# Optimization experiments

Measured on AMD Instinct MI355X. Metric: run time of the kernel, lower is better.

Reference implementation:

```python
import jax, jax.numpy as jnp
import numpy as np

B, C, H, I = 32, 8, 512, 512


def act(x):
    # CustomActivation == hardtanh: (|x+1| - |x-1|) / 2
    return (jnp.abs(x + 1.0) - jnp.abs(x - 1.0)) * 0.5


def setup_inputs() -> dict:
    key = jax.random.key(0)
    ks = jax.random.split(key, 12)
    inp = jax.random.normal(ks[0], (B, C, H, I), dtype=jnp.float32)
    p_mask = jax.random.normal(ks[1], (H, I), dtype=jnp.float32)
    # Wp: tril(randn) with diagonal filled to 1 (matches __init__ + the no_grad
    # tril/clamp projection in forward, which is a no-op right after init).
    Wp = jnp.tril(jax.random.normal(ks[2], (H, H), dtype=jnp.float32))
    Wp = Wp - jnp.diag(jnp.diag(Wp)) + jnp.eye(H, dtype=jnp.float32)
    Wp_diag = jnp.ones((H,), dtype=jnp.float32)
    Wzp = jax.random.normal(ks[3], (H, H), dtype=jnp.float32)
    s = 1.0 / np.sqrt(I)
    def lin(k):
        kw, kb = jax.random.split(k)
        W = jax.random.uniform(kw, (I, I), jnp.float32, -s, s)
        b = jax.random.uniform(kb, (I,), jnp.float32, -s, s)
        return W, b
    p_lin_w, p_lin_b = lin(ks[4])
    z_lin_w, z_lin_b = lin(ks[5])
    fc1_w, fc1_b = lin(ks[6])
    fc2_w, fc2_b = lin(ks[7])
    return {
        'input': inp, 'p_mask': p_mask, 'Wp': Wp, 'Wp_diag': Wp_diag, 'Wzp': Wzp,
        'p_lin_w': p_lin_w, 'p_lin_b': p_lin_b,
        'z_lin_w': z_lin_w, 'z_lin_b': z_lin_b,
        'fc1_w': fc1_w, 'fc1_b': fc1_b, 'fc2_w': fc2_w, 'fc2_b': fc2_b,
    }


def reference(input, p_mask, Wp, Wp_diag, Wzp,
              p_lin_w, p_lin_b, z_lin_w, z_lin_b,
              fc1_w, fc1_b, fc2_w, fc2_b):
    x = input * (1.0 / 5000.0)                      # [B,C,H,I]
    p_set = x * act(p_mask)                         # split_input, broadcast over B,C
    Wp_eff = Wp + jnp.diag(Wp_diag)                 # [H,H]
    # per-channel Wp @ p_set[c], batched over B and C in one GEMM
    tp = jnp.einsum('hk,bcki->bchi', Wp_eff, p_set)
    tp = act(act(tp) @ p_lin_w.T + p_lin_b)         # p_output_layer
    tz = jnp.einsum('hk,bchi->bchi', Wzp, tp)       # wait-free channel-batched GEMM
    tz = act(act(tz) @ z_lin_w.T + z_lin_b)         # z_output_layer
    # sum over in_channel (out_channel==1 so broadcast-accumulate == sum)
    combined = tp.sum(axis=1) + tz.sum(axis=1) + x[:, 0]  # [B,H,I]
    out = jax.nn.relu(combined @ fc1_w.T + fc1_b)
    out = out @ fc2_w.T + fc2_b
    return out
```

## Files before the change

### kernel.cpp

```cpp
#include <hip/hip_runtime.h>

namespace {

constexpr int Bn = 32, Cn = 8, Hn = 512, In = 512;
constexpr size_t HI = (size_t)Hn * In;
constexpr float SC = 1.0f / 5000.0f;

using s16x8 = __attribute__((ext_vector_type(8))) short;
using f32x4 = __attribute__((ext_vector_type(4))) float;

__device__ __forceinline__ float actf(float x) {
    return fminf(1.0f, fmaxf(-1.0f, x));
}

__device__ __forceinline__ unsigned short f2bf(float f) {
    unsigned u = __builtin_bit_cast(unsigned, f);
    u += 0x7FFFu + ((u >> 16) & 1u);
    return (unsigned short)(u >> 16);
}
__device__ __forceinline__ float bf2f(unsigned short h) {
    return __builtin_bit_cast(float, (unsigned)h << 16);
}

__device__ __forceinline__ void async16(const void* g, void* l) {
    __builtin_amdgcn_global_load_lds(
        (const __attribute__((address_space(1))) unsigned*)g,
        (__attribute__((address_space(3))) unsigned*)l, 16, 0, 0);
}

template<int EPI, bool PCOL, bool TRI>
__global__ __launch_bounds__(256, 3) void mfma_gemm(
    const unsigned short* __restrict__ A,
    const unsigned short* __restrict__ Bt,
    const float* __restrict__ bias,
    const float* __restrict__ zrow,
    unsigned short* __restrict__ out0,
    unsigned short* __restrict__ out1,
    float* __restrict__ outf,
    size_t sB, size_t sC)
{
    __shared__ __align__(16) unsigned short As[128 * 32];
    __shared__ __align__(16) unsigned short Bs[128 * 32];

    const int tid  = threadIdx.x;
    const int wid  = tid >> 6, lane = tid & 63;
    const int wr   = wid >> 1, wc = wid & 1;

    const int bid = blockIdx.x;
    const int p = ((bid >> 5) << 3) | (bid & 7);
    const int q = (bid >> 3) & 3;
    const int rt = PCOL ? q : p;
    const int ct = PCOL ? (p & 3) : q;
    const size_t zb = PCOL ? (size_t)(p >> 2) : 0;

    const char* Ab = (const char*)A + (size_t)rt * 131072;
    const char* Bb = (const char*)(Bt + zb * sB) + (size_t)ct * 131072;

    f32x4 acc[4][4] = {};

    const int o0  = tid * 16;
    const int r0s = o0 >> 6;
    const int c0s = o0 & 63;

    const int kSteps = TRI ? (rt + 1) * 4 : 16;

    for (int ks = 0; ks < kSteps; ++ks) {
        const int k0b = ks * 64;
        async16(Ab + (size_t)r0s * 1024 + k0b + c0s,        (char*)As + wid * 1024);
        async16(Ab + (size_t)(64 + r0s) * 1024 + k0b + c0s, (char*)As + 4096 + wid * 1024);
        async16(Bb + (size_t)r0s * 1024 + k0b + c0s,        (char*)Bs + wid * 1024);
        async16(Bb + (size_t)(64 + r0s) * 1024 + k0b + c0s, (char*)Bs + 4096 + wid * 1024);
        __syncthreads();

        s16x8 a[4], b[4];
        const int kc = (lane >> 4) * 16;
        const int ar = wr * 64 + (lane & 15);
        const int br = wc * 64 + (lane & 15);
        #pragma unroll
        for (int m = 0; m < 4; ++m)
            a[m] = *(const s16x8*)((const char*)As + (size_t)(ar + m * 16) * 64 + kc);
        #pragma unroll
        for (int n = 0; n < 4; ++n)
            b[n] = *(const s16x8*)((const char*)Bs + (size_t)(br + n * 16) * 64 + kc);
        #pragma unroll
        for (int m = 0; m < 4; ++m)
            #pragma unroll
            for (int n = 0; n < 4; ++n)
                acc[m][n] = __builtin_amdgcn_mfma_f32_16x16x32_bf16(a[m], b[n], acc[m][n], 0, 0, 0);
        __syncthreads();
    }

    const int cb = ct * 128 + wc * 64 + (lane & 15);
    const int rb = rt * 128 + wr * 64 + ((lane >> 4) << 2);
    #pragma unroll
    for (int m = 0; m < 4; ++m) {
        #pragma unroll
        for (int n = 0; n < 4; ++n) {
            const int c = cb + n * 16;
            #pragma unroll
            for (int j = 0; j < 4; ++j) {
                const int r = rb + m * 16 + j;
                float v = acc[m][n][j];
                const size_t idx = zb * sC + (size_t)r * 512 + c;
                if (EPI == 0) {
                    out0[idx] = f2bf(actf(v));
                } else if (EPI == 1) {
                    float tp = actf(v + bias[c]);
                    out0[idx] = f2bf(tp);
                    out1[idx] = f2bf(actf(zrow[r & 511] * tp));
                } else if (EPI == 2) {
                    out0[idx] = f2bf(actf(v + bias[c]));
                } else if (EPI == 3) {
                    out0[idx] = f2bf(fmaxf(v + bias[c], 0.0f));
                } else {
                    outf[idx] = v + bias[c];
                }
            }
        }
    }
}

__global__ __launch_bounds__(256) void reduce_both(
    const unsigned short* __restrict__ tp,
    const unsigned short* __restrict__ tz,
    const float* __restrict__ x0,
    unsigned short* __restrict__ comb)
{
    size_t idx = (size_t)blockIdx.x * 256 + threadIdx.x;
    size_t b = idx >> 16;
    size_t p = (idx & 65535) * 4;
    float4 xv = *(const float4*)&x0[(b * Cn) * HI + p];
    float s0 = xv.x * SC, s1 = xv.y * SC, s2 = xv.z * SC, s3 = xv.w * SC;
    #pragma unroll
    for (int c = 0; c < Cn; ++c) {
        size_t q = (b * Cn + c) * HI + p;
        ushort4 a = *(const ushort4*)&tp[q];
        ushort4 d = *(const ushort4*)&tz[q];
        s0 += bf2f(a.x) + bf2f(d.x);
        s1 += bf2f(a.y) + bf2f(d.y);
        s2 += bf2f(a.z) + bf2f(d.z);
        s3 += bf2f(a.w) + bf2f(d.w);
    }
    ushort4 o;
    o.x = f2bf(s0); o.y = f2bf(s1); o.z = f2bf(s2); o.w = f2bf(s3);
    *(ushort4*)&comb[b * HI + p] = o;
}

__global__ __launch_bounds__(256) void transpose_mask(
    const float* __restrict__ x, const float* __restrict__ mask,
    unsigned short* __restrict__ xst)
{
    __shared__ float t[64][65];
    const int bc = blockIdx.z;
    const int i0 = blockIdx.x * 64, k0 = blockIdx.y * 64;
    const int r4 = threadIdx.x >> 6, cc = threadIdx.x & 63;
    const float* xp = x + (size_t)bc * HI;
    #pragma unroll
    for (int it = 0; it < 16; ++it) {
        int kl = it * 4 + r4;
        size_t g = (size_t)(k0 + kl) * In + i0 + cc;
        t[kl][cc] = xp[g] * (actf(mask[g]) * SC);
    }
    __syncthreads();
    unsigned short* op = xst + (size_t)bc * HI;
    #pragma unroll
    for (int it = 0; it < 16; ++it) {
        int il = it * 4 + r4;
        op[(size_t)(i0 + il) * Hn + k0 + cc] = f2bf(t[cc][il]);
    }
}

__global__ __launch_bounds__(256) void prep_wpe_bf(
    const float* __restrict__ Wp, const float* __restrict__ Wpd,
    unsigned short* __restrict__ o)
{
    int idx = blockIdx.x * 256 + threadIdx.x;
    int i = idx >> 9, j = idx & 511;
    o[idx] = f2bf(Wp[idx] + (i == j ? Wpd[i] : 0.0f));
}

__global__ __launch_bounds__(256) void conv_bf(
    const float* __restrict__ s, unsigned short* __restrict__ o)
{
    int idx = blockIdx.x * 256 + threadIdx.x;
    o[idx] = f2bf(s[idx]);
}

__global__ __launch_bounds__(64) void rowsum(
    const float* __restrict__ W, float* __restrict__ zr)
{
    int h = blockIdx.x, l = threadIdx.x;
    float s = 0.0f;
    for (int k = l; k < Hn; k += 64) s += W[h * Hn + k];
    #pragma unroll
    for (int off = 32; off; off >>= 1) s += __shfl_down(s, off, 64);
    if (!l) zr[h] = s;
}

}

extern "C" void kernel_launch(void* const* d_in, const int* in_sizes, int n_in,
                              void* d_out, int out_size, void* d_ws, size_t ws_size,
                              hipStream_t stream)
{
    const float* input  = (const float*)d_in[0];
    const float* p_mask = (const float*)d_in[1];
    const float* Wp     = (const float*)d_in[2];
    const float* Wpd    = (const float*)d_in[3];
    const float* Wzp    = (const float*)d_in[4];
    const float* plw    = (const float*)d_in[5];
    const float* plb    = (const float*)d_in[6];
    const float* zlw    = (const float*)d_in[7];
    const float* zlb    = (const float*)d_in[8];
    const float* f1w    = (const float*)d_in[9];
    const float* f1b    = (const float*)d_in[10];
    const float* f2w    = (const float*)d_in[11];
    const float* f2b    = (const float*)d_in[12];

    constexpr size_t WB = 512 * 512 * 2;
    char* w = (char*)d_ws;
    auto alloc = [&](size_t bytes) { char* p = w; w += (bytes + 255) & ~255ull; return p; };

    unsigned short* Wpeb  = (unsigned short*)alloc(WB);
    unsigned short* plwb  = (unsigned short*)alloc(WB);
    unsigned short* zlwb  = (unsigned short*)alloc(WB);
    unsigned short* f1wb  = (unsigned short*)alloc(WB);
    unsigned short* f2wb  = (unsigned short*)alloc(WB);
    float*          zrw   = (float*)alloc(512 * 4);
    unsigned short* combb = (unsigned short*)alloc((size_t)Bn * HI * 2);
    unsigned short* out1  = (unsigned short*)alloc((size_t)Bn * HI * 2);

    size_t fixedB = (size_t)(w - (char*)d_ws);
    int chunk = 32;
    while (chunk > 1 &&
           fixedB + 4ull * (size_t)chunk * Cn * HI * 2 + 4096 > ws_size)
        chunk >>= 1;
    const size_t CB = (size_t)chunk * Cn * HI * 2;
    unsigned short* xst   = (unsigned short*)alloc(CB);
    unsigned short* tpact = (unsigned short*)alloc(CB);
    unsigned short* tpb   = (unsigned short*)alloc(CB);
    unsigned short* tzin  = (unsigned short*)alloc(CB);
    unsigned short* tzb   = xst;

    prep_wpe_bf<<<512 * 512 / 256, 256, 0, stream>>>(Wp, Wpd, Wpeb);
    conv_bf<<<1024, 256, 0, stream>>>(plw, plwb);
    conv_bf<<<1024, 256, 0, stream>>>(zlw, zlwb);
    conv_bf<<<1024, 256, 0, stream>>>(f1w, f1wb);
    conv_bf<<<1024, 256, 0, stream>>>(f2w, f2wb);
    rowsum<<<512, 64, 0, stream>>>(Wzp, zrw);

    for (int b0 = 0; b0 < Bn; b0 += chunk) {
        const int nc = chunk * Cn;
        const float* inp_c = input + (size_t)b0 * Cn * HI;

        transpose_mask<<<dim3(8, 8, nc), 256, 0, stream>>>(inp_c, p_mask, xst);
        mfma_gemm<0, true, true><<<nc * 16, 256, 0, stream>>>(
            Wpeb, xst, nullptr, nullptr, tpact, nullptr, nullptr, HI, HI);
        mfma_gemm<1, false, false><<<nc * 16, 256, 0, stream>>>(
            tpact, plwb, plb, zrw, tpb, tzin, nullptr, 0, 0);
        mfma_gemm<2, false, false><<<nc * 16, 256, 0, stream>>>(
            tzin, zlwb, zlb, nullptr, tzb, nullptr, nullptr, 0, 0);
        reduce_both<<<chunk * 256, 256, 0, stream>>>(
            tpb, tzb, inp_c, combb + (size_t)b0 * HI);
    }

    mfma_gemm<3, false, false><<<512, 256, 0, stream>>>(
        combb, f1wb, f1b, nullptr, out1, nullptr, nullptr, 0, 0);
    mfma_gemm<4, false, false><<<512, 256, 0, stream>>>(
        out1, f2wb, f2b, nullptr, nullptr, nullptr, (float*)d_out, 0, 0);
}
```

Measured before the change: 564.3 us.

## Double-buffer LDS tiles in MFMA GEMM and relayout for conflict-free reads

Replaces the single-buffered load/sync/compute loop with two LDS buffers. The next K-step's async global-to-LDS loads are issued before the current step's MFMAs, and the kernel waits with an explicit vmcnt(0) plus a barrier. The LDS layout changes to K-chunk-major 16-byte rows, so each fragment read is contiguous per lane quarter, which should reduce bank conflicts. LDS use doubles to 32KB per block, which may limit occupancy under launch_bounds(256,3). The loop steps two K-steps at a time, so it relies on kSteps being even.

Measured after the change: 728.3 us. 29.1% more time.

```diff
diff --git a/kernel.cpp b/kernel.cpp
--- a/kernel.cpp
+++ b/kernel.cpp
@@ -27,6 +27,8 @@
         (const __attribute__((address_space(1))) unsigned*)g,
         (__attribute__((address_space(3))) unsigned*)l, 16, 0, 0);
 }
+
+#define VMCNT0 asm volatile("s_waitcnt vmcnt(0)" ::: "memory")
 
 template<int EPI, bool PCOL, bool TRI>
 __global__ __launch_bounds__(256, 3) void mfma_gemm(
@@ -39,12 +41,13 @@
     float* __restrict__ outf,
     size_t sB, size_t sC)
 {
-    __shared__ __align__(16) unsigned short As[128 * 32];
-    __shared__ __align__(16) unsigned short Bs[128 * 32];
+    __shared__ __align__(16) char lds0[16384];
+    __shared__ __align__(16) char lds1[16384];
 
     const int tid  = threadIdx.x;
     const int wid  = tid >> 6, lane = tid & 63;
     const int wr   = wid >> 1, wc = wid & 1;
+    const int l15  = lane & 15, kq = lane >> 4;
 
     const int bid = blockIdx.x;
     const int p = ((bid >> 5) << 3) | (bid & 7);
@@ -58,40 +61,52 @@
 
     f32x4 acc[4][4] = {};
 
-    const int o0  = tid * 16;
-    const int r0s = o0 >> 6;
-    const int c0s = o0 & 63;
-
-    const int kSteps = TRI ? (rt + 1) * 4 : 16;
-
-    for (int ks = 0; ks < kSteps; ++ks) {
-        const int k0b = ks * 64;
-        async16(Ab + (size_t)r0s * 1024 + k0b + c0s,        (char*)As + wid * 1024);
-        async16(Ab + (size_t)(64 + r0s) * 1024 + k0b + c0s, (char*)As + 4096 + wid * 1024);
-        async16(Bb + (size_t)r0s * 1024 + k0b + c0s,        (char*)Bs + wid * 1024);
-        async16(Bb + (size_t)(64 + r0s) * 1024 + k0b + c0s, (char*)Bs + 4096 + wid * 1024);
-        __syncthreads();
-
+    const size_t ro = (size_t)(tid & 127) * 1024;
+    const int    hi16 = (tid >> 7) * 16;
+    auto stage_ab = [&](char* buf, int k0b) {
+        const int kb = k0b + hi16;
+        async16(Ab + ro + kb,      buf + tid * 16);
+        async16(Ab + ro + kb + 32, buf + 4096 + tid * 16);
+        async16(Bb + ro + kb,      buf + 8192 + tid * 16);
+        async16(Bb + ro + kb + 32, buf + 12288 + tid * 16);
+    };
+
+    auto compute = [&](const char* buf) {
         s16x8 a[4], b[4];
-        const int kc = (lane >> 4) * 16;
-        const int ar = wr * 64 + (lane & 15);
-        const int br = wc * 64 + (lane & 15);
+        const int ko = kq * 2048;
         #pragma unroll
         for (int m = 0; m < 4; ++m)
-            a[m] = *(const s16x8*)((const char*)As + (size_t)(ar + m * 16) * 64 + kc);
+            a[m] = *(const s16x8*)(buf + ko + (wr * 64 + m * 16 + l15) * 16);
         #pragma unroll
         for (int n = 0; n < 4; ++n)
-            b[n] = *(const s16x8*)((const char*)Bs + (size_t)(br + n * 16) * 64 + kc);
+            b[n] = *(const s16x8*)(buf + 8192 + ko + (wc * 64 + n * 16 + l15) * 16);
         #pragma unroll
         for (int m = 0; m < 4; ++m)
             #pragma unroll
             for (int n = 0; n < 4; ++n)
                 acc[m][n] = __builtin_amdgcn_mfma_f32_16x16x32_bf16(a[m], b[n], acc[m][n], 0, 0, 0);
-        __syncthreads();
-    }
-
-    const int cb = ct * 128 + wc * 64 + (lane & 15);
-    const int rb = rt * 128 + wr * 64 + ((lane >> 4) << 2);
+    };
+
+    const int kSteps = TRI ? (rt + 1) * 4 : 16;
+
+    stage_ab(lds0, 0);
+    VMCNT0;
+    __builtin_amdgcn_s_barrier();
+
+    #pragma unroll 1
+    for (int ks = 0; ks < kSteps; ks += 2) {
+        stage_ab(lds1, (ks + 1) * 64);
+        compute(lds0);
+        VMCNT0;
+        __builtin_amdgcn_s_barrier();
+        if (ks + 2 < kSteps) stage_ab(lds0, (ks + 2) * 64);
+        compute(lds1);
+        VMCNT0;
+        __builtin_amdgcn_s_barrier();
+    }
+
+    const int cb = ct * 128 + wc * 64 + l15;
+    const int rb = rt * 128 + wr * 64 + (kq << 2);
     #pragma unroll
     for (int m = 0; m < 4; ++m) {
         #pragma unroll
```
